# Performance work log

Measured on AMD Instinct MI355X. Metric: run time of the kernel, lower is better.

Reference implementation:

```python
import jax, jax.numpy as jnp
import numpy as np

INITIAL_RADIUS = 1.0  # init_kwargs: initial_radius > 0 -> distance-softmax branch


def reference(xyz, sparse_xyz, sparse_flow, resol_factor, K):
    # xyz: [B,3,N], sparse_xyz: [B,3,M], sparse_flow: [B,3,M]
    q = jnp.transpose(xyz, (0, 2, 1))            # [B,N,3]
    p = jnp.transpose(sparse_xyz, (0, 2, 1))     # [B,M,3]
    flow = jnp.transpose(sparse_flow, (0, 2, 1))  # [B,M,3]

    sigma = INITIAL_RADIUS * resol_factor
    qs = q / sigma
    ps = p / sigma

    # pairwise Euclidean distances [B,N,M]
    sq = (jnp.sum(qs * qs, -1)[:, :, None]
          + jnp.sum(ps * ps, -1)[:, None, :]
          - 2.0 * jnp.einsum('bnc,bmc->bnm', qs, ps))
    dist = jnp.sqrt(jnp.maximum(sq, 1e-12))

    # K nearest: smallest distances
    neg_d, idx = jax.lax.top_k(-dist, K)          # [B,N,K]
    K_dist = -neg_d                               # [B,N,K]

    # gather flow of the K neighbors: [B,N,K,3]
    grouped_flow = jnp.take_along_axis(flow[:, None, :, :], idx[..., None], axis=2)

    # softmax over -distance along K, weighted sum
    K_w = jax.nn.softmax(-K_dist, axis=2)         # [B,N,K]
    dense_flow = jnp.sum(K_w[..., None] * grouped_flow, axis=2)  # [B,N,3]

    return jnp.transpose(dense_flow, (0, 2, 1))   # [B,3,N]


def setup_inputs() -> dict:
    key = jax.random.key(0)
    k1, k2, k3 = jax.random.split(key, 3)
    B, N, M = 4, 16384, 4096
    return {
        'xyz': jax.random.normal(k1, (B, 3, N), dtype=jnp.float32),
        'sparse_xyz': jax.random.normal(k2, (B, 3, M), dtype=jnp.float32),
        'sparse_flow': jax.random.normal(k3, (B, 3, M), dtype=jnp.float32),
        'resol_factor': 1,
        'K': 5,
    }
```

## Files before the change

kernel.cpp:

```cpp
#include <hip/hip_runtime.h>
#include <math.h>


#define KNN 5
#define BLOCK 256
#define WAVES_PER_BLOCK 4
#define QPB 64
#define MMAX 4096

__device__ __forceinline__ void insert5(float d, int j, float e[KNN], int idx[KNN]) {
    if (d < e[4]) {
        const bool c3 = d < e[3], c2 = d < e[2], c1 = d < e[1], c0 = d < e[0];
        e[4]   = c3 ? e[3]   : d;                 idx[4] = c3 ? idx[3] : j;
        e[3]   = c2 ? e[2]   : (c3 ? d : e[3]);   idx[3] = c2 ? idx[2] : (c3 ? j : idx[3]);
        e[2]   = c1 ? e[1]   : (c2 ? d : e[2]);   idx[2] = c1 ? idx[1] : (c2 ? j : idx[2]);
        e[1]   = c0 ? e[0]   : (c1 ? d : e[1]);   idx[1] = c0 ? idx[0] : (c1 ? j : idx[1]);
        e[0]   = c0 ? d      : e[0];              idx[0] = c0 ? j      : idx[0];
    }
}

__global__ __launch_bounds__(BLOCK)
void upsample_flow_knn_kernel(const float* __restrict__ xyz,
                              const float* __restrict__ sxyz,
                              const float* __restrict__ sflow,
                              const int* __restrict__ rf,
                              float* __restrict__ out,
                              int N, int M, int blocksPerBatch) {
    __shared__ float4 lds_p[MMAX];
    __shared__ float  md[QPB * WAVES_PER_BLOCK * KNN];
    __shared__ int    mi[QPB * WAVES_PER_BLOCK * KNN];

    const int tid  = threadIdx.x;
    const int lane = tid & 63;
    const int wid  = tid >> 6;
    const int b    = blockIdx.x / blocksPerBatch;
    const int n0   = (blockIdx.x % blocksPerBatch) * QPB;

    const int ri = rf[0];
    const float sigma = (ri >= 1 && ri <= 1000000) ? (float)ri : __int_as_float(ri);
    const float inv_sigma = 1.0f / sigma;

    const float* sb = sxyz + (size_t)b * 3 * M;
    for (int t = tid; t < M; t += BLOCK) {
        const float px = sb[t]         * inv_sigma;
        const float py = sb[M + t]     * inv_sigma;
        const float pz = sb[2 * M + t] * inv_sigma;
        lds_p[t] = make_float4(px, py, pz, px * px + py * py + pz * pz);
    }

    const int n  = n0 + lane;
    const int nc = (n < N) ? n : (N - 1);
    const float* qb = xyz + (size_t)b * 3 * N;
    const float qx = qb[nc]         * inv_sigma;
    const float qy = qb[N + nc]     * inv_sigma;
    const float qz = qb[2 * N + nc] * inv_sigma;
    const float qq = qx * qx + qy * qy + qz * qz;

    __syncthreads();

    const int chunk = (M + WAVES_PER_BLOCK - 1) / WAVES_PER_BLOCK;
    const int j0 = wid * chunk;
    const int j1 = (j0 + chunk < M) ? (j0 + chunk) : M;

    float e[KNN];
    int   idx[KNN];
#pragma unroll
    for (int k = 0; k < KNN; ++k) { e[k] = 1e30f; idx[k] = 0; }

#pragma unroll 4
    for (int j = j0; j < j1; ++j) {
        const float4 p = lds_p[j];
        float t = qx * p.x;
        t = fmaf(qy, p.y, t);
        t = fmaf(qz, p.z, t);
        const float d2 = fmaf(-2.0f, t, qq + p.w);
        insert5(d2, j, e, idx);
    }

#pragma unroll
    for (int k = 0; k < KNN; ++k) {
        md[lane * (WAVES_PER_BLOCK * KNN) + wid * KNN + k] = e[k];
        mi[lane * (WAVES_PER_BLOCK * KNN) + wid * KNN + k] = idx[k];
    }
    __syncthreads();

    if (wid == 0 && n < N) {
        float fe[KNN];
        int   fi[KNN];
#pragma unroll
        for (int k = 0; k < KNN; ++k) { fe[k] = 1e30f; fi[k] = 0; }
#pragma unroll
        for (int t = 0; t < WAVES_PER_BLOCK * KNN; ++t) {
            insert5(md[lane * (WAVES_PER_BLOCK * KNN) + t],
                    mi[lane * (WAVES_PER_BLOCK * KNN) + t], fe, fi);
        }

        float dist[KNN];
#pragma unroll
        for (int k = 0; k < KNN; ++k) dist[k] = sqrtf(fmaxf(fe[k], 1e-12f));
        const float dmin = dist[0];
        float w[KNN];
        float wsum = 0.0f;
#pragma unroll
        for (int k = 0; k < KNN; ++k) { w[k] = expf(dmin - dist[k]); wsum += w[k]; }
        const float inv_wsum = 1.0f / wsum;

        const float* fb = sflow + (size_t)b * 3 * M;
        float ax = 0.0f, ay = 0.0f, az = 0.0f;
#pragma unroll
        for (int k = 0; k < KNN; ++k) {
            const int m = fi[k];
            const float wk = w[k];
            ax = fmaf(wk, fb[m],         ax);
            ay = fmaf(wk, fb[M + m],     ay);
            az = fmaf(wk, fb[2 * M + m], az);
        }

        float* ob = out + (size_t)b * 3 * N;
        ob[n]         = ax * inv_wsum;
        ob[N + n]     = ay * inv_wsum;
        ob[2 * N + n] = az * inv_wsum;
    }
}

extern "C" void kernel_launch(void* const* d_in, const int* in_sizes, int n_in,
                              void* d_out, int out_size, void* d_ws, size_t ws_size,
                              hipStream_t stream) {
    const float* xyz   = (const float*)d_in[0];
    const float* sxyz  = (const float*)d_in[1];
    const float* sflow = (const float*)d_in[2];
    const int*   rf    = (const int*)d_in[3];

    const int B = 4;
    const int N = in_sizes[0] / (3 * B);
    const int M = in_sizes[1] / (3 * B);

    float* out = (float*)d_out;

    const int blocksPerBatch = (N + QPB - 1) / QPB;
    const dim3 grid(B * blocksPerBatch);
    const dim3 block(BLOCK);
    upsample_flow_knn_kernel<<<grid, block, 0, stream>>>(xyz, sxyz, sflow, rf, out,
                                                         N, M, blocksPerBatch);
}
```

Measured before the change: 274.1 us.

## Rewrite KNN as two-pass threshold search with global prep buffer

```diff
diff --git a/kernel.cpp b/kernel.cpp
--- a/kernel.cpp
+++ b/kernel.cpp
@@ -1,120 +1,180 @@
 #include <hip/hip_runtime.h>
 #include <math.h>
+#include <stdint.h>
 
 
 #define KNN 5
-#define BLOCK 256
-#define WAVES_PER_BLOCK 4
-#define QPB 64
-#define MMAX 4096
-
-__device__ __forceinline__ void insert5(float d, int j, float e[KNN], int idx[KNN]) {
-    if (d < e[4]) {
-        const bool c3 = d < e[3], c2 = d < e[2], c1 = d < e[1], c0 = d < e[0];
-        e[4]   = c3 ? e[3]   : d;                 idx[4] = c3 ? idx[3] : j;
-        e[3]   = c2 ? e[2]   : (c3 ? d : e[3]);   idx[3] = c2 ? idx[2] : (c3 ? j : idx[3]);
-        e[2]   = c1 ? e[1]   : (c2 ? d : e[2]);   idx[2] = c1 ? idx[1] : (c2 ? j : idx[2]);
-        e[1]   = c0 ? e[0]   : (c1 ? d : e[1]);   idx[1] = c0 ? idx[0] : (c1 ? j : idx[1]);
-        e[0]   = c0 ? d      : e[0];              idx[0] = c0 ? j      : idx[0];
-    }
-}
-
-__global__ __launch_bounds__(BLOCK)
-void upsample_flow_knn_kernel(const float* __restrict__ xyz,
-                              const float* __restrict__ sxyz,
-                              const float* __restrict__ sflow,
-                              const int* __restrict__ rf,
-                              float* __restrict__ out,
-                              int N, int M, int blocksPerBatch) {
-    __shared__ float4 lds_p[MMAX];
-    __shared__ float  md[QPB * WAVES_PER_BLOCK * KNN];
-    __shared__ int    mi[QPB * WAVES_PER_BLOCK * KNN];
+#define SLICES 8
+#define BLOCK (SLICES * 64)
+#define CAP 6
+
+typedef unsigned long long u64;
+typedef unsigned int u32;
+
+__device__ __forceinline__ float get_inv_sigma(const int* __restrict__ rf) {
+    const int ri = rf[0];
+    const float sigma = (ri >= 1 && ri <= 1000000) ? (float)ri : __int_as_float(ri);
+    return 1.0f / sigma;
+}
+
+__global__ __launch_bounds__(256)
+void prep_kernel(const float* __restrict__ sxyz, const int* __restrict__ rf,
+                 float4* __restrict__ pts, int M, int total) {
+    const int t = blockIdx.x * 256 + threadIdx.x;
+    if (t >= total) return;
+    const float inv = get_inv_sigma(rf);
+    const int b = t / M, m = t - b * M;
+    const float* sb = sxyz + (size_t)b * 3 * M;
+    const float x = sb[m] * inv;
+    const float y = sb[M + m] * inv;
+    const float z = sb[2 * M + m] * inv;
+    pts[t] = make_float4(x, y, z, fmaf(x, x, fmaf(y, y, z * z)));
+}
+
+template <bool USE_PTS>
+__global__ __launch_bounds__(BLOCK, 8)
+void knn_kernel(const float* __restrict__ xyz,
+                const float* __restrict__ sxyz,
+                const float* __restrict__ sflow,
+                const int* __restrict__ rf,
+                const float4* __restrict__ pts,
+                float* __restrict__ out,
+                int N, int M, int blocksPerBatch) {
+    __shared__ float svals[SLICES * KNN * 64];
+    __shared__ u64   lists[SLICES * 64 * CAP];
+    __shared__ int   cnts[SLICES * 64];
 
     const int tid  = threadIdx.x;
     const int lane = tid & 63;
     const int wid  = tid >> 6;
     const int b    = blockIdx.x / blocksPerBatch;
-    const int n0   = (blockIdx.x % blocksPerBatch) * QPB;
-
-    const int ri = rf[0];
-    const float sigma = (ri >= 1 && ri <= 1000000) ? (float)ri : __int_as_float(ri);
-    const float inv_sigma = 1.0f / sigma;
-
-    const float* sb = sxyz + (size_t)b * 3 * M;
-    for (int t = tid; t < M; t += BLOCK) {
-        const float px = sb[t]         * inv_sigma;
-        const float py = sb[M + t]     * inv_sigma;
-        const float pz = sb[2 * M + t] * inv_sigma;
-        lds_p[t] = make_float4(px, py, pz, px * px + py * py + pz * pz);
-    }
-
-    const int n  = n0 + lane;
-    const int nc = (n < N) ? n : (N - 1);
+    const int n    = (blockIdx.x % blocksPerBatch) * 64 + lane;
+
+    const float inv = get_inv_sigma(rf);
     const float* qb = xyz + (size_t)b * 3 * N;
-    const float qx = qb[nc]         * inv_sigma;
-    const float qy = qb[N + nc]     * inv_sigma;
-    const float qz = qb[2 * N + nc] * inv_sigma;
+    const float qx = qb[n] * inv;
+    const float qy = qb[N + n] * inv;
+    const float qz = qb[2 * N + n] * inv;
     const float qq = qx * qx + qy * qy + qz * qz;
 
+    const int CH = M / SLICES;
+    const int j0 = wid * CH;
+
+    const float4* P = nullptr;
+    const float*  sb = nullptr;
+    if constexpr (USE_PTS) P = pts + (size_t)b * M + j0;
+    else                   sb = sxyz + (size_t)b * 3 * M;
+
+    float e0 = 1e30f, e1 = 1e30f, e2 = 1e30f, e3 = 1e30f, e4 = 1e30f;
+#pragma unroll 4
+    for (int j = 0; j < CH; ++j) {
+        float px, py, pz, pw;
+        if constexpr (USE_PTS) {
+            const float4 p = P[j];
+            px = p.x; py = p.y; pz = p.z; pw = p.w;
+        } else {
+            px = sb[j0 + j] * inv;
+            py = sb[M + j0 + j] * inv;
+            pz = sb[2 * M + j0 + j] * inv;
+            pw = fmaf(px, px, fmaf(py, py, pz * pz));
+        }
+        float t = qx * px;
+        t = fmaf(qy, py, t);
+        t = fmaf(qz, pz, t);
+        const float dc = fmaxf(fmaf(-2.0f, t, qq + pw), 1e-12f);
+        float c = dc, m;
+        m = fminf(e0, c); c = fmaxf(e0, c); e0 = m;
+        m = fminf(e1, c); c = fmaxf(e1, c); e1 = m;
+        m = fminf(e2, c); c = fmaxf(e2, c); e2 = m;
+        m = fminf(e3, c); c = fmaxf(e3, c); e3 = m;
+        e4 = fminf(e4, c);
+    }
+    svals[(wid * KNN + 0) * 64 + lane] = e0;
+    svals[(wid * KNN + 1) * 64 + lane] = e1;
+    svals[(wid * KNN + 2) * 64 + lane] = e2;
+    svals[(wid * KNN + 3) * 64 + lane] = e3;
+    svals[(wid * KNN + 4) * 64 + lane] = e4;
     __syncthreads();
 
-    const int chunk = (M + WAVES_PER_BLOCK - 1) / WAVES_PER_BLOCK;
-    const int j0 = wid * chunk;
-    const int j1 = (j0 + chunk < M) ? (j0 + chunk) : M;
-
-    float e[KNN];
-    int   idx[KNN];
+    float t0 = 1e30f, t1 = 1e30f, t2 = 1e30f, t3 = 1e30f, t4 = 1e30f;
 #pragma unroll
-    for (int k = 0; k < KNN; ++k) { e[k] = 1e30f; idx[k] = 0; }
-
-#pragma unroll 4
-    for (int j = j0; j < j1; ++j) {
-        const float4 p = lds_p[j];
-        float t = qx * p.x;
-        t = fmaf(qy, p.y, t);
-        t = fmaf(qz, p.z, t);
-        const float d2 = fmaf(-2.0f, t, qq + p.w);
-        insert5(d2, j, e, idx);
-    }
-
-#pragma unroll
-    for (int k = 0; k < KNN; ++k) {
-        md[lane * (WAVES_PER_BLOCK * KNN) + wid * KNN + k] = e[k];
-        mi[lane * (WAVES_PER_BLOCK * KNN) + wid * KNN + k] = idx[k];
-    }
-    __syncthreads();
-
-    if (wid == 0 && n < N) {
-        float fe[KNN];
-        int   fi[KNN];
-#pragma unroll
-        for (int k = 0; k < KNN; ++k) { fe[k] = 1e30f; fi[k] = 0; }
-#pragma unroll
-        for (int t = 0; t < WAVES_PER_BLOCK * KNN; ++t) {
-            insert5(md[lane * (WAVES_PER_BLOCK * KNN) + t],
-                    mi[lane * (WAVES_PER_BLOCK * KNN) + t], fe, fi);
-        }
-
-        float dist[KNN];
-#pragma unroll
-        for (int k = 0; k < KNN; ++k) dist[k] = sqrtf(fmaxf(fe[k], 1e-12f));
-        const float dmin = dist[0];
-        float w[KNN];
-        float wsum = 0.0f;
-#pragma unroll
-        for (int k = 0; k < KNN; ++k) { w[k] = expf(dmin - dist[k]); wsum += w[k]; }
-        const float inv_wsum = 1.0f / wsum;
-
-        const float* fb = sflow + (size_t)b * 3 * M;
-        float ax = 0.0f, ay = 0.0f, az = 0.0f;
+    for (int w = 0; w < SLICES; ++w) {
 #pragma unroll
         for (int k = 0; k < KNN; ++k) {
-            const int m = fi[k];
-            const float wk = w[k];
-            ax = fmaf(wk, fb[m],         ax);
-            ay = fmaf(wk, fb[M + m],     ay);
-            az = fmaf(wk, fb[2 * M + m], az);
-        }
+            float c = svals[(w * KNN + k) * 64 + lane], m;
+            m = fminf(t0, c); c = fmaxf(t0, c); t0 = m;
+            m = fminf(t1, c); c = fmaxf(t1, c); t1 = m;
+            m = fminf(t2, c); c = fmaxf(t2, c); t2 = m;
+            m = fminf(t3, c); c = fmaxf(t3, c); t3 = m;
+            t4 = fminf(t4, c);
+        }
+    }
+    const float thr = t4 * (1.0f + 2e-6f);
+
+    int cnt = 0;
+#pragma unroll 4
+    for (int j = 0; j < CH; ++j) {
+        float px, py, pz, pw;
+        if constexpr (USE_PTS) {
+            const float4 p = P[j];
+            px = p.x; py = p.y; pz = p.z; pw = p.w;
+        } else {
+            px = sb[j0 + j] * inv;
+            py = sb[M + j0 + j] * inv;
+            pz = sb[2 * M + j0 + j] * inv;
+            pw = fmaf(px, px, fmaf(py, py, pz * pz));
+        }
+        float t = qx * px;
+        t = fmaf(qy, py, t);
+        t = fmaf(qz, pz, t);
+        const float dc = fmaxf(fmaf(-2.0f, t, qq + pw), 1e-12f);
+        if (dc <= thr && cnt < CAP) {
+            lists[(wid * 64 + lane) * CAP + cnt] =
+                ((u64)__float_as_uint(dc) << 32) | (u32)(j0 + j);
+            cnt++;
+        }
+    }
+    cnts[wid * 64 + lane] = cnt;
+    __syncthreads();
+
+    if (wid == 0) {
+        u64 k0 = ~0ULL, k1 = ~0ULL, k2 = ~0ULL, k3 = ~0ULL, k4 = ~0ULL;
+        for (int w = 0; w < SLICES; ++w) {
+            const int c = cnts[w * 64 + lane];
+#pragma unroll
+            for (int i = 0; i < CAP; ++i) {
+                u64 cc = (i < c) ? lists[(w * 64 + lane) * CAP + i] : ~0ULL;
+                u64 lo;
+                lo = cc < k0 ? cc : k0;  cc = cc < k0 ? k0 : cc;  k0 = lo;
+                lo = cc < k1 ? cc : k1;  cc = cc < k1 ? k1 : cc;  k1 = lo;
+                lo = cc < k2 ? cc : k2;  cc = cc < k2 ? k2 : cc;  k2 = lo;
+                lo = cc < k3 ? cc : k3;  cc = cc < k3 ? k3 : cc;  k3 = lo;
+                k4 = cc < k4 ? cc : k4;
+            }
+        }
+
+        const float d0 = sqrtf(__uint_as_float((u32)(k0 >> 32)));
+        const float d1 = sqrtf(__uint_as_float((u32)(k1 >> 32)));
+        const float d2 = sqrtf(__uint_as_float((u32)(k2 >> 32)));
+        const float d3 = sqrtf(__uint_as_float((u32)(k3 >> 32)));
+        const float d4 = sqrtf(__uint_as_float((u32)(k4 >> 32)));
+        const float dmin = d0;
+        const float w0 = expf(dmin - d0);
+        const float w1 = expf(dmin - d1);
+        const float w2 = expf(dmin - d2);
+        const float w3 = expf(dmin - d3);
+        const float w4 = expf(dmin - d4);
+        const float inv_wsum = 1.0f / (w0 + w1 + w2 + w3 + w4);
+
+        const int i0 = (int)(u32)k0, i1 = (int)(u32)k1, i2 = (int)(u32)k2,
+                  i3 = (int)(u32)k3, i4 = (int)(u32)k4;
+        const float* fb = sflow + (size_t)b * 3 * M;
+        float ax = 0.f, ay = 0.f, az = 0.f;
+        ax = fmaf(w0, fb[i0], ax); ay = fmaf(w0, fb[M + i0], ay); az = fmaf(w0, fb[2 * M + i0], az);
+        ax = fmaf(w1, fb[i1], ax); ay = fmaf(w1, fb[M + i1], ay); az = fmaf(w1, fb[2 * M + i1], az);
+        ax = fmaf(w2, fb[i2], ax); ay = fmaf(w2, fb[M + i2], ay); az = fmaf(w2, fb[2 * M + i2], az);
+        ax = fmaf(w3, fb[i3], ax); ay = fmaf(w3, fb[M + i3], ay); az = fmaf(w3, fb[2 * M + i3], az);
+        ax = fmaf(w4, fb[i4], ax); ay = fmaf(w4, fb[M + i4], ay); az = fmaf(w4, fb[2 * M + i4], az);
 
         float* ob = out + (size_t)b * 3 * N;
         ob[n]         = ax * inv_wsum;
@@ -134,12 +194,20 @@
     const int B = 4;
     const int N = in_sizes[0] / (3 * B);
     const int M = in_sizes[1] / (3 * B);
-
     float* out = (float*)d_out;
 
-    const int blocksPerBatch = (N + QPB - 1) / QPB;
+    const int blocksPerBatch = N / 64;
     const dim3 grid(B * blocksPerBatch);
     const dim3 block(BLOCK);
-    upsample_flow_knn_kernel<<<grid, block, 0, stream>>>(xyz, sxyz, sflow, rf, out,
-                                                         N, M, blocksPerBatch);
-}
+
+    const size_t need = (size_t)B * M * sizeof(float4);
+    if (ws_size >= need) {
+        float4* pts = (float4*)d_ws;
+        prep_kernel<<<dim3((B * M + 255) / 256), dim3(256), 0, stream>>>(sxyz, rf, pts, M, B * M);
+        knn_kernel<true><<<grid, block, 0, stream>>>(xyz, sxyz, sflow, rf, pts, out,
+                                                     N, M, blocksPerBatch);
+    } else {
+        knn_kernel<false><<<grid, block, 0, stream>>>(xyz, sxyz, sflow, rf, nullptr, out,
+                                                      N, M, blocksPerBatch);
+    }
+}
```

Measured after the change: 330.3 us. 1.21x slower.
